# Kernel tuning notes

Hardware: AMD Instinct MI355X
Metric: run time of the kernel (lower is better)

## Reference

```python
import jax, jax.numpy as jnp
import numpy as np

B, T, C, H = 4, 4096, 1024, 64


def setup_inputs() -> dict:
    key = jax.random.key(0)
    ks = jax.random.split(key, 7)
    s = C ** -0.5
    return {
        "x": jax.random.normal(ks[0], (B, T, C), dtype=jnp.float32),
        "Wk": jax.random.normal(ks[1], (C, H), dtype=jnp.float32) * s,
        "bk": jax.random.normal(ks[2], (H,), dtype=jnp.float32) * 0.02,
        "Wq": jax.random.normal(ks[3], (C, H), dtype=jnp.float32) * s,
        "bq": jax.random.normal(ks[4], (H,), dtype=jnp.float32) * 0.02,
        "Wv": jax.random.normal(ks[5], (C, H), dtype=jnp.float32) * s,
        "bv": jax.random.normal(ks[6], (H,), dtype=jnp.float32) * 0.02,
    }


def reference(x, Wk, bk, Wq, bq, Wv, bv):
    Bx, Tx, Cx = x.shape
    k = x @ Wk + bk            # [B,T,H]
    q = x @ Wq + bq            # [B,T,H]
    v = x @ Wv + bv            # [B,T,H]
    scale = Cx ** -0.5         # NOTE: source scales by n_embed^-0.5, not head_size
    # Faithful to source: scores = K @ Q^T (rows indexed by key position)
    wei = jnp.einsum("bth,bsh->bts", k, q) * scale  # [B,T,T]
    causal = jnp.tril(jnp.ones((Tx, Tx), dtype=bool))
    wei = jnp.where(causal, wei, -jnp.inf)
    wei = jax.nn.softmax(wei, axis=-1)
    out = jnp.einsum("bts,bsh->bth", wei, v)        # [B,T,H]
    return out
```

## Files before the change

kernel.cpp:

```cpp
#include <hip/hip_runtime.h>
#include <hip/hip_bf16.h>
#include <math.h>


typedef __attribute__((ext_vector_type(8))) short bf16x8;
typedef __attribute__((ext_vector_type(4))) short bf16x4;
typedef __attribute__((ext_vector_type(4))) float f32x4;

#define MFMA16(a, b, c) __builtin_amdgcn_mfma_f32_16x16x32_bf16(a, b, c, 0, 0, 0)

__device__ __forceinline__ short f2bf(float f) {
    union { float f; unsigned u; } v; v.f = f;
    unsigned r = v.u + 0x7FFFu + ((v.u >> 16) & 1u);
    return (short)(r >> 16);
}

static constexpr int T = 4096;
static constexpr int C = 1024;
static constexpr int H = 64;
static constexpr int BATCH = 4;
static constexpr int M = BATCH * T;
static constexpr int CPB = 288;
static constexpr float LOG2E = 1.44269504088896340736f;
static constexpr float KSCALE = 0.03125f * LOG2E;

__global__ __launch_bounds__(256) void wtrans_zero_kernel(
    const float* __restrict__ Wk, const float* __restrict__ Wq,
    const float* __restrict__ Wv, short* __restrict__ Wt_g,
    float* __restrict__ out, float* __restrict__ lP)
{
    const int blk = blockIdx.x;
    const int tid = threadIdx.x;
    if (blk < 48) {
        __shared__ short Wl[64][72];
        const int mat = blk / 16, k0 = (blk % 16) * 64;
        const float* W = (mat == 0) ? Wk : (mat == 1) ? Wq : Wv;
        const int hr = (tid & 15) * 4, kr = tid >> 4;
        #pragma unroll
        for (int pass = 0; pass < 4; ++pass) {
            int k = kr + pass * 16;
            float4 v = *(const float4*)&W[(size_t)(k0 + k) * H + hr];
            Wl[hr + 0][k] = f2bf(v.x);
            Wl[hr + 1][k] = f2bf(v.y);
            Wl[hr + 2][k] = f2bf(v.z);
            Wl[hr + 3][k] = f2bf(v.w);
        }
        __syncthreads();
        const int h = tid >> 2, kk = (tid & 3) * 16;
        bf16x8 o0 = *(const bf16x8*)&Wl[h][kk];
        bf16x8 o1 = *(const bf16x8*)&Wl[h][kk + 8];
        *(bf16x8*)&Wt_g[(size_t)(mat * 64 + h) * C + k0 + kk] = o0;
        *(bf16x8*)&Wt_g[(size_t)(mat * 64 + h) * C + k0 + kk + 8] = o1;
    } else if (blk < 304) {
        const float4 z = {0.f, 0.f, 0.f, 0.f};
        float4* o4 = (float4*)out;
        const int idx = (blk - 48) * 256 + tid;
        #pragma unroll
        for (int i = 0; i < 4; ++i) o4[idx + i * 65536] = z;
    } else {
        const float4 z = {0.f, 0.f, 0.f, 0.f};
        float4* l4 = (float4*)lP;
        #pragma unroll
        for (int i = 0; i < 16; ++i) l4[tid + i * 256] = z;
    }
}

__global__ __launch_bounds__(512) void proj_kernel(
    const float* __restrict__ x, const short* __restrict__ Wt_g,
    const float* __restrict__ bk, const float* __restrict__ bq,
    const float* __restrict__ bv,
    short* __restrict__ Kb, short* __restrict__ Qb, short* __restrict__ Vt)
{
    __shared__ short As[2][64][72];
    __shared__ short Ws[2][192][72];
    const int tid = threadIdx.x;
    const int wv = tid >> 6, lane = tid & 63, quad = lane >> 4, l16 = lane & 15;
    const int grp = wv >> 2, w4 = wv & 3;
    const int m0 = blockIdx.x * 64;
    const int arow = tid >> 3, ac8 = (tid & 7) * 8;

    f32x4 acc[6];
    #pragma unroll
    for (int i = 0; i < 6; ++i)
        for (int j = 0; j < 4; ++j) acc[i][j] = 0.f;

    float4 xa0, xa1;
    bf16x8 wl[3];
    auto gload = [&](int k0) {
        xa0 = *(const float4*)&x[(size_t)(m0 + arow) * C + k0 + ac8];
        xa1 = *(const float4*)&x[(size_t)(m0 + arow) * C + k0 + ac8 + 4];
        #pragma unroll
        for (int i = 0; i < 3; ++i) {
            int idx = tid + i * 512;
            wl[i] = *(const bf16x8*)&Wt_g[(size_t)(idx >> 3) * C + k0 + (idx & 7) * 8];
        }
    };
    auto lwrite = [&](int p) {
        bf16x8 av;
        av[0] = f2bf(xa0.x); av[1] = f2bf(xa0.y); av[2] = f2bf(xa0.z); av[3] = f2bf(xa0.w);
        av[4] = f2bf(xa1.x); av[5] = f2bf(xa1.y); av[6] = f2bf(xa1.z); av[7] = f2bf(xa1.w);
        *(bf16x8*)&As[p][arow][ac8] = av;
        #pragma unroll
        for (int i = 0; i < 3; ++i) {
            int idx = tid + i * 512;
            *(bf16x8*)&Ws[p][idx >> 3][(idx & 7) * 8] = wl[i];
        }
    };

    gload(0);
    lwrite(0);
    __syncthreads();
    for (int it = 0; it < 16; ++it) {
        const int p = it & 1;
        if (it < 15) gload((it + 1) * 64);
        bf16x8 a0 = *(const bf16x8*)&As[p][w4 * 16 + l16][quad * 8];
        bf16x8 a1 = *(const bf16x8*)&As[p][w4 * 16 + l16][32 + quad * 8];
        #pragma unroll
        for (int tn = 0; tn < 6; ++tn) {
            bf16x8 b0 = *(const bf16x8*)&Ws[p][grp * 96 + tn * 16 + l16][quad * 8];
            bf16x8 b1 = *(const bf16x8*)&Ws[p][grp * 96 + tn * 16 + l16][32 + quad * 8];
            acc[tn] = MFMA16(a0, b0, acc[tn]);
            acc[tn] = MFMA16(a1, b1, acc[tn]);
        }
        if (it < 15) {
            lwrite((it + 1) & 1);
            __syncthreads();
        }
    }
    #pragma unroll
    for (int tn = 0; tn < 6; ++tn) {
        int gc = grp * 96 + tn * 16 + l16;
        int mat = gc >> 6, h = gc & 63;
        const float* bias = (mat == 0) ? bk : (mat == 1) ? bq : bv;
        float bb = bias[h];
        float sc = (mat == 0) ? KSCALE : 1.f;
        #pragma unroll
        for (int r = 0; r < 4; ++r) {
            int row = m0 + w4 * 16 + quad * 4 + r;
            short val = f2bf((acc[tn][r] + bb) * sc);
            if (mat == 0)      Kb[(size_t)row * H + h] = val;
            else if (mat == 1) Qb[(size_t)row * H + h] = val;
            else               Vt[((size_t)(row >> 6)) * 4096 + h * 64 + (row & 63)] = val;
        }
    }
}

__device__ __forceinline__ void chunk_map8(int c, int& tt, int& chunk) {
    int k = 1;
    while (c >= 4 * k * (k + 1)) ++k;
    int off = c - 4 * k * (k - 1);
    int q = off / k;
    tt = 8 * (k - 1) + q;
    chunk = off - q * k;
}

__global__ __launch_bounds__(256) void attn_part_kernel(
    const short* __restrict__ Kb, const short* __restrict__ Qb,
    const short* __restrict__ Vt, float* __restrict__ out,
    float* __restrict__ lP)
{
    __shared__ short Pl[4][2][16][76];
    __shared__ float Ob[64][66];
    __shared__ float lnb[64];
    const int tid = threadIdx.x;
    const int wv = tid >> 6, lane = tid & 63;
    const int quad = lane >> 4, l16 = lane & 15;
    const int sp = wv & 1, sh = wv >> 1;
    const int g = blockIdx.x;
    const int b = g & 3;
    const int c = CPB - 1 - (g >> 2);
    int tt, chunk;
    chunk_map8(c, tt, chunk);
    const int t0 = tt * 64;
    const int sA = sp * 2, sB = sp * 2 + 1;
    const int st0 = chunk * 8;
    const int st1 = min(st0 + 8, tt + 1);
    const size_t base = (size_t)b * T * H;

    const short* krA = Kb + base + (size_t)(t0 + sA * 16 + l16) * H;
    const short* krB = Kb + base + (size_t)(t0 + sB * 16 + l16) * H;
    bf16x8 kf0a = *(const bf16x8*)(krA + quad * 8);
    bf16x8 kf1a = *(const bf16x8*)(krA + 32 + quad * 8);
    bf16x8 kf0b = *(const bf16x8*)(krB + quad * 8);
    bf16x8 kf1b = *(const bf16x8*)(krB + 32 + quad * 8);

    bf16x8 ones;
    #pragma unroll
    for (int j = 0; j < 8; ++j) ones[j] = (short)0x3F80;

    f32x4 oA[4], oB[4], lnA, lnB;
    #pragma unroll
    for (int i = 0; i < 4; ++i)
        for (int j = 0; j < 4; ++j) { oA[i][j] = 0.f; oB[i][j] = 0.f; }
    #pragma unroll
    for (int j = 0; j < 4; ++j) { lnA[j] = 0.f; lnB[j] = 0.f; }

    const int myb = st0 + sh;
    const short* qp = Qb + base + (size_t)(myb * 64 + l16) * H + quad * 8;
    const short* vp = Vt + ((size_t)(b * 64 + myb)) * 4096 + l16 * 64 + quad * 8;

    bf16x8 qc0[4], qc1[4];
    if (myb < st1) {
        #pragma unroll
        for (int tn = 0; tn < 4; ++tn) {
            qc0[tn] = *(const bf16x8*)(qp + tn * 1024);
            qc1[tn] = *(const bf16x8*)(qp + tn * 1024 + 32);
        }
    }

    for (int st = myb; st < st1; st += 2) {
        bf16x8 vb0[4], vb1[4];
        #pragma unroll
        for (int hn = 0; hn < 4; ++hn) {
            vb0[hn] = *(const bf16x8*)(vp + hn * 1024);
            vb1[hn] = *(const bf16x8*)(vp + hn * 1024 + 32);
        }
        f32x4 sAc[4], sBc[4];
        #pragma unroll
        for (int tn = 0; tn < 4; ++tn) {
            #pragma unroll
            for (int j = 0; j < 4; ++j) { sAc[tn][j] = 0.f; sBc[tn][j] = 0.f; }
            sAc[tn] = MFMA16(qc0[tn], kf0a, sAc[tn]);
            sAc[tn] = MFMA16(qc1[tn], kf1a, sAc[tn]);
            sBc[tn] = MFMA16(qc0[tn], kf0b, sBc[tn]);
            sBc[tn] = MFMA16(qc1[tn], kf1b, sBc[tn]);
        }
        const size_t qoff = (st + 2 < st1) ? 8192 : 0;
        #pragma unroll
        for (int tn = 0; tn < 4; ++tn) {
            qc0[tn] = *(const bf16x8*)(qp + qoff + tn * 1024);
            qc1[tn] = *(const bf16x8*)(qp + qoff + tn * 1024 + 32);
        }
        const bool diag = (st == tt);
        #pragma unroll
        for (int tn = 0; tn < 4; ++tn) {
            bf16x4 pa, pb;
            #pragma unroll
            for (int r = 0; r < 4; ++r) {
                float va = sAc[tn][r], vb = sBc[tn][r];
                if (diag) {
                    int scol = tn * 16 + quad * 4 + r;
                    if (scol > sA * 16 + l16) va = -INFINITY;
                    if (scol > sB * 16 + l16) vb = -INFINITY;
                }
                pa[r] = f2bf(exp2f(va));
                pb[r] = f2bf(exp2f(vb));
            }
            *(bf16x4*)&Pl[wv][0][l16][tn * 16 + quad * 4] = pa;
            *(bf16x4*)&Pl[wv][1][l16][tn * 16 + quad * 4] = pb;
        }
        bf16x8 aA0 = *(const bf16x8*)&Pl[wv][0][l16][quad * 8];
        bf16x8 aA1 = *(const bf16x8*)&Pl[wv][0][l16][32 + quad * 8];
        bf16x8 aB0 = *(const bf16x8*)&Pl[wv][1][l16][quad * 8];
        bf16x8 aB1 = *(const bf16x8*)&Pl[wv][1][l16][32 + quad * 8];
        #pragma unroll
        for (int hn = 0; hn < 4; ++hn) {
            oA[hn] = MFMA16(aA0, vb0[hn], oA[hn]);
            oA[hn] = MFMA16(aA1, vb1[hn], oA[hn]);
            oB[hn] = MFMA16(aB0, vb0[hn], oB[hn]);
            oB[hn] = MFMA16(aB1, vb1[hn], oB[hn]);
        }
        lnA = MFMA16(aA0, ones, lnA);
        lnA = MFMA16(aA1, ones, lnA);
        lnB = MFMA16(aB0, ones, lnB);
        lnB = MFMA16(aB1, ones, lnB);
        qp += 8192;
        vp += 8192;
    }

    const int rbase = sp * 32;
    if (sh == 1) {
        #pragma unroll
        for (int hn = 0; hn < 4; ++hn)
            #pragma unroll
            for (int r = 0; r < 4; ++r) {
                Ob[rbase + quad * 4 + r][hn * 16 + l16] = oA[hn][r];
                Ob[rbase + 16 + quad * 4 + r][hn * 16 + l16] = oB[hn][r];
            }
        if (l16 == 0) {
            #pragma unroll
            for (int r = 0; r < 4; ++r) {
                lnb[rbase + quad * 4 + r] = lnA[r];
                lnb[rbase + 16 + quad * 4 + r] = lnB[r];
            }
        }
    }
    __syncthreads();
    if (sh == 0) {
        #pragma unroll
        for (int hn = 0; hn < 4; ++hn)
            #pragma unroll
            for (int r = 0; r < 4; ++r) {
                int ra = t0 + rbase + quad * 4 + r;
                int rb = ra + 16;
                float va = oA[hn][r] + Ob[rbase + quad * 4 + r][hn * 16 + l16];
                float vb = oB[hn][r] + Ob[rbase + 16 + quad * 4 + r][hn * 16 + l16];
                atomicAdd(&out[base + (size_t)ra * H + hn * 16 + l16], va);
                atomicAdd(&out[base + (size_t)rb * H + hn * 16 + l16], vb);
            }
        if (l16 == 0) {
            #pragma unroll
            for (int r = 0; r < 4; ++r) {
                atomicAdd(&lP[b * T + t0 + rbase + quad * 4 + r],
                          lnA[r] + lnb[rbase + quad * 4 + r]);
                atomicAdd(&lP[b * T + t0 + rbase + 16 + quad * 4 + r],
                          lnB[r] + lnb[rbase + 16 + quad * 4 + r]);
            }
        }
    }
}

__global__ __launch_bounds__(256) void norm_kernel(
    float* __restrict__ out, const float* __restrict__ lP)
{
    const int i = blockIdx.x * 256 + threadIdx.x;
    float4 v = ((const float4*)out)[i];
    const float inv = 1.f / lP[i >> 4];
    v.x *= inv; v.y *= inv; v.z *= inv; v.w *= inv;
    ((float4*)out)[i] = v;
}

extern "C" void kernel_launch(void* const* d_in, const int* in_sizes, int n_in,
                              void* d_out, int out_size, void* d_ws, size_t ws_size,
                              hipStream_t stream) {
    const float* x  = (const float*)d_in[0];
    const float* Wk = (const float*)d_in[1];
    const float* bk = (const float*)d_in[2];
    const float* Wq = (const float*)d_in[3];
    const float* bq = (const float*)d_in[4];
    const float* Wv = (const float*)d_in[5];
    const float* bv = (const float*)d_in[6];
    float* out = (float*)d_out;

    char* ws = (char*)d_ws;
    size_t off = 0;
    short* Kb   = (short*)(ws + off); off += (size_t)M * H * 2;
    short* Qb   = (short*)(ws + off); off += (size_t)M * H * 2;
    short* Vt   = (short*)(ws + off); off += (size_t)M * H * 2;
    short* Wt_g = (short*)(ws + off); off += (size_t)192 * C * 2;
    float* lP   = (float*)(ws + off); off += (size_t)M * 4;

    wtrans_zero_kernel<<<305, 256, 0, stream>>>(Wk, Wq, Wv, Wt_g, out, lP);
    proj_kernel<<<M / 64, 512, 0, stream>>>(x, Wt_g, bk, bq, bv, Kb, Qb, Vt);
    attn_part_kernel<<<BATCH * CPB, 256, 0, stream>>>(Kb, Qb, Vt, out, lP);
    norm_kernel<<<M * H / 4 / 256, 256, 0, stream>>>(out, lP);
}
```

Before: 180.2 us.

## Replace atomic partial accumulation with per-chunk partial buffers and a reduction kernel

```diff
diff --git a/kernel.cpp b/kernel.cpp
--- a/kernel.cpp
+++ b/kernel.cpp
@@ -24,45 +24,31 @@
 static constexpr float LOG2E = 1.44269504088896340736f;
 static constexpr float KSCALE = 0.03125f * LOG2E;
 
-__global__ __launch_bounds__(256) void wtrans_zero_kernel(
+__global__ __launch_bounds__(256) void wtrans_kernel(
     const float* __restrict__ Wk, const float* __restrict__ Wq,
-    const float* __restrict__ Wv, short* __restrict__ Wt_g,
-    float* __restrict__ out, float* __restrict__ lP)
+    const float* __restrict__ Wv, short* __restrict__ Wt_g)
 {
     const int blk = blockIdx.x;
     const int tid = threadIdx.x;
-    if (blk < 48) {
-        __shared__ short Wl[64][72];
-        const int mat = blk / 16, k0 = (blk % 16) * 64;
-        const float* W = (mat == 0) ? Wk : (mat == 1) ? Wq : Wv;
-        const int hr = (tid & 15) * 4, kr = tid >> 4;
-        #pragma unroll
-        for (int pass = 0; pass < 4; ++pass) {
-            int k = kr + pass * 16;
-            float4 v = *(const float4*)&W[(size_t)(k0 + k) * H + hr];
-            Wl[hr + 0][k] = f2bf(v.x);
-            Wl[hr + 1][k] = f2bf(v.y);
-            Wl[hr + 2][k] = f2bf(v.z);
-            Wl[hr + 3][k] = f2bf(v.w);
-        }
-        __syncthreads();
-        const int h = tid >> 2, kk = (tid & 3) * 16;
-        bf16x8 o0 = *(const bf16x8*)&Wl[h][kk];
-        bf16x8 o1 = *(const bf16x8*)&Wl[h][kk + 8];
-        *(bf16x8*)&Wt_g[(size_t)(mat * 64 + h) * C + k0 + kk] = o0;
-        *(bf16x8*)&Wt_g[(size_t)(mat * 64 + h) * C + k0 + kk + 8] = o1;
-    } else if (blk < 304) {
-        const float4 z = {0.f, 0.f, 0.f, 0.f};
-        float4* o4 = (float4*)out;
-        const int idx = (blk - 48) * 256 + tid;
-        #pragma unroll
-        for (int i = 0; i < 4; ++i) o4[idx + i * 65536] = z;
-    } else {
-        const float4 z = {0.f, 0.f, 0.f, 0.f};
-        float4* l4 = (float4*)lP;
-        #pragma unroll
-        for (int i = 0; i < 16; ++i) l4[tid + i * 256] = z;
-    }
+    __shared__ short Wl[64][72];
+    const int mat = blk / 16, k0 = (blk % 16) * 64;
+    const float* W = (mat == 0) ? Wk : (mat == 1) ? Wq : Wv;
+    const int hr = (tid & 15) * 4, kr = tid >> 4;
+    #pragma unroll
+    for (int pass = 0; pass < 4; ++pass) {
+        int k = kr + pass * 16;
+        float4 v = *(const float4*)&W[(size_t)(k0 + k) * H + hr];
+        Wl[hr + 0][k] = f2bf(v.x);
+        Wl[hr + 1][k] = f2bf(v.y);
+        Wl[hr + 2][k] = f2bf(v.z);
+        Wl[hr + 3][k] = f2bf(v.w);
+    }
+    __syncthreads();
+    const int h = tid >> 2, kk = (tid & 3) * 16;
+    bf16x8 o0 = *(const bf16x8*)&Wl[h][kk];
+    bf16x8 o1 = *(const bf16x8*)&Wl[h][kk + 8];
+    *(bf16x8*)&Wt_g[(size_t)(mat * 64 + h) * C + k0 + kk] = o0;
+    *(bf16x8*)&Wt_g[(size_t)(mat * 64 + h) * C + k0 + kk + 8] = o1;
 }
 
 __global__ __launch_bounds__(512) void proj_kernel(
@@ -156,8 +142,8 @@
 
 __global__ __launch_bounds__(256) void attn_part_kernel(
     const short* __restrict__ Kb, const short* __restrict__ Qb,
-    const short* __restrict__ Vt, float* __restrict__ out,
-    float* __restrict__ lP)
+    const short* __restrict__ Vt, float* __restrict__ Pb,
+    float* __restrict__ lnPb)
 {
     __shared__ short Pl[4][2][16][76];
     __shared__ float Ob[64][66];
@@ -287,37 +273,67 @@
     }
     __syncthreads();
     if (sh == 0) {
+        float* Pc = Pb + (size_t)(b * CPB + c) * 4096;
         #pragma unroll
         for (int hn = 0; hn < 4; ++hn)
             #pragma unroll
             for (int r = 0; r < 4; ++r) {
-                int ra = t0 + rbase + quad * 4 + r;
+                int ra = rbase + quad * 4 + r;
                 int rb = ra + 16;
-                float va = oA[hn][r] + Ob[rbase + quad * 4 + r][hn * 16 + l16];
-                float vb = oB[hn][r] + Ob[rbase + 16 + quad * 4 + r][hn * 16 + l16];
-                atomicAdd(&out[base + (size_t)ra * H + hn * 16 + l16], va);
-                atomicAdd(&out[base + (size_t)rb * H + hn * 16 + l16], vb);
+                float va = oA[hn][r] + Ob[ra][hn * 16 + l16];
+                float vb = oB[hn][r] + Ob[rb][hn * 16 + l16];
+                Pc[(size_t)ra * 64 + hn * 16 + l16] = va;
+                Pc[(size_t)rb * 64 + hn * 16 + l16] = vb;
             }
         if (l16 == 0) {
-            #pragma unroll
-            for (int r = 0; r < 4; ++r) {
-                atomicAdd(&lP[b * T + t0 + rbase + quad * 4 + r],
-                          lnA[r] + lnb[rbase + quad * 4 + r]);
-                atomicAdd(&lP[b * T + t0 + rbase + 16 + quad * 4 + r],
-                          lnB[r] + lnb[rbase + 16 + quad * 4 + r]);
-            }
-        }
-    }
-}
-
-__global__ __launch_bounds__(256) void norm_kernel(
-    float* __restrict__ out, const float* __restrict__ lP)
+            float* lc = lnPb + (size_t)(b * CPB + c) * 64;
+            #pragma unroll
+            for (int r = 0; r < 4; ++r) {
+                lc[rbase + quad * 4 + r] = lnA[r] + lnb[rbase + quad * 4 + r];
+                lc[rbase + 16 + quad * 4 + r] = lnB[r] + lnb[rbase + 16 + quad * 4 + r];
+            }
+        }
+    }
+}
+
+__global__ __launch_bounds__(256) void reduce_norm_kernel(
+    const float* __restrict__ Pb, const float* __restrict__ lnPb,
+    float* __restrict__ out)
 {
-    const int i = blockIdx.x * 256 + threadIdx.x;
-    float4 v = ((const float4*)out)[i];
-    const float inv = 1.f / lP[i >> 4];
-    v.x *= inv; v.y *= inv; v.z *= inv; v.w *= inv;
-    ((float4*)out)[i] = v;
+    const int blk = blockIdx.x;
+    const int b = blk >> 6, tt = blk & 63;
+    const int k = tt / 8 + 1;
+    const int base_c = 4 * k * (k - 1) + (tt - 8 * (k - 1)) * k;
+    const int tid = threadIdx.x;
+    __shared__ float lnS[64];
+    if (tid < 64) {
+        float s = 0.f;
+        for (int i = 0; i < k; ++i)
+            s += lnPb[(size_t)(b * CPB + base_c + i) * 64 + tid];
+        lnS[tid] = 1.f / s;
+    }
+    __syncthreads();
+    float4 acc[4];
+    #pragma unroll
+    for (int j = 0; j < 4; ++j) acc[j] = {0.f, 0.f, 0.f, 0.f};
+    for (int i = 0; i < k; ++i) {
+        const float4* p4 = (const float4*)(Pb + (size_t)(b * CPB + base_c + i) * 4096);
+        #pragma unroll
+        for (int j = 0; j < 4; ++j) {
+            float4 v = p4[tid + j * 256];
+            acc[j].x += v.x; acc[j].y += v.y; acc[j].z += v.z; acc[j].w += v.w;
+        }
+    }
+    float4* o4 = (float4*)out;
+    const size_t obase = ((size_t)b * T + tt * 64) * 16;
+    #pragma unroll
+    for (int j = 0; j < 4; ++j) {
+        int idx = tid + j * 256;
+        float inv = lnS[idx >> 4];
+        float4 v = acc[j];
+        v.x *= inv; v.y *= inv; v.z *= inv; v.w *= inv;
+        o4[obase + idx] = v;
+    }
 }
 
 extern "C" void kernel_launch(void* const* d_in, const int* in_sizes, int n_in,
@@ -338,10 +354,11 @@
     short* Qb   = (short*)(ws + off); off += (size_t)M * H * 2;
     short* Vt   = (short*)(ws + off); off += (size_t)M * H * 2;
     short* Wt_g = (short*)(ws + off); off += (size_t)192 * C * 2;
-    float* lP   = (float*)(ws + off); off += (size_t)M * 4;
-
-    wtrans_zero_kernel<<<305, 256, 0, stream>>>(Wk, Wq, Wv, Wt_g, out, lP);
+    float* Pb   = (float*)(ws + off); off += (size_t)BATCH * CPB * 4096 * 4;
+    float* lnPb = (float*)(ws + off); off += (size_t)BATCH * CPB * 64 * 4;
+
+    wtrans_kernel<<<48, 256, 0, stream>>>(Wk, Wq, Wv, Wt_g);
     proj_kernel<<<M / 64, 512, 0, stream>>>(x, Wt_g, bk, bq, bv, Kb, Qb, Vt);
-    attn_part_kernel<<<BATCH * CPB, 256, 0, stream>>>(Kb, Qb, Vt, out, lP);
-    norm_kernel<<<M * H / 4 / 256, 256, 0, stream>>>(out, lP);
-}
+    attn_part_kernel<<<BATCH * CPB, 256, 0, stream>>>(Kb, Qb, Vt, Pb, lnPb);
+    reduce_norm_kernel<<<BATCH * 64, 256, 0, stream>>>(Pb, lnPb, out);
+}
```

After: 179.7 us. No clear change (-0.3%).
